# Kernel tuning notes

Measured on AMD Instinct MI355X. Metric: run time of the kernel, lower is better.

## Reference

```python
import jax, jax.numpy as jnp
import numpy as np

TEMPERATURE = 0.5


def setup_inputs() -> dict:
    key = jax.random.key(0)
    k1, k2 = jax.random.split(key)
    B, D = 8192, 128
    z_i = jax.random.normal(k1, (B, D), dtype=jnp.float32)
    z_j = jax.random.normal(k2, (B, D), dtype=jnp.float32)
    return {"z_i": z_i, "z_j": z_j}


def reference(z_i, z_j):
    B = z_i.shape[0]
    eps = 1e-12  # matches torch F.normalize default clamp
    zi = z_i / jnp.maximum(jnp.linalg.norm(z_i, axis=1, keepdims=True), eps)
    zj = z_j / jnp.maximum(jnp.linalg.norm(z_j, axis=1, keepdims=True), eps)
    reps = jnp.concatenate([zi, zj], axis=0)  # [2B, D], unit rows
    # cosine similarity of unit vectors == dot product -> single GEMM
    sim = reps @ reps.T  # [2B, 2B]
    n = 2 * B
    diag = jnp.eye(n, dtype=bool)
    sim = jnp.where(diag, -1e9, sim) / TEMPERATURE
    labels = jnp.concatenate([jnp.arange(B) + B, jnp.arange(B)])  # positive pair indices
    logp = jax.nn.log_softmax(sim, axis=1)
    loss = -jnp.mean(jnp.take_along_axis(logp, labels[:, None], axis=1))
    return loss
```

## Files before the change

### kernel.cpp

```cpp
#include <hip/hip_runtime.h>
#include <hip/hip_bf16.h>

#define NB 8192
#define ND 128
#define N2 16384

#define CPB 512
#define CTILE 64
#define NT (CPB / CTILE)
#define TILEB (CTILE * 128)

typedef __attribute__((ext_vector_type(4))) float f32x4;
typedef __attribute__((ext_vector_type(4))) int v4i;
typedef __attribute__((ext_vector_type(8))) int v8i;

static constexpr float SQRT_C_VAL = 1.69864368f;

__global__ __launch_bounds__(256) void nrm_kernel(const float* __restrict__ zi,
                                                  const float* __restrict__ zj,
                                                  unsigned short* __restrict__ reps8_u16,
                                                  float* __restrict__ pos,
                                                  float* __restrict__ ssum,
                                                  float* __restrict__ sdiag) {
    const int gtid = blockIdx.x * 256 + threadIdx.x;
    if (gtid < N2) ssum[gtid] = 0.f;
    const int pair = gtid >> 6;
    const int lane = threadIdx.x & 63;
    const float2 vi = *reinterpret_cast<const float2*>(zi + pair * ND + lane * 2);
    const float2 vj = *reinterpret_cast<const float2*>(zj + pair * ND + lane * 2);
    float ssi = vi.x * vi.x + vi.y * vi.y;
    float ssj = vj.x * vj.x + vj.y * vj.y;
#pragma unroll
    for (int m = 1; m < 64; m <<= 1) {
        ssi += __shfl_xor(ssi, m);
        ssj += __shfl_xor(ssj, m);
    }
    float ni = fmaxf(sqrtf(ssi), 1e-12f);
    float nj = fmaxf(sqrtf(ssj), 1e-12f);
    const float ii = 1.0f / ni, ij = 1.0f / nj;
    const float uix = vi.x * ii, uiy = vi.y * ii;
    const float ujx = vj.x * ij, ujy = vj.y * ij;
    float d = uix * ujx + uiy * ujy;
#pragma unroll
    for (int m = 1; m < 64; m <<= 1) d += __shfl_xor(d, m);
    if (lane == 0) pos[pair] = d;
    const int pki = __builtin_amdgcn_cvt_pk_fp8_f32(uix * SQRT_C_VAL, uiy * SQRT_C_VAL, 0, false);
    const int pkj = __builtin_amdgcn_cvt_pk_fp8_f32(ujx * SQRT_C_VAL, ujy * SQRT_C_VAL, 0, false);
    reps8_u16[pair * 64 + lane] = (unsigned short)(pki & 0xFFFF);
    reps8_u16[(NB + pair) * 64 + lane] = (unsigned short)(pkj & 0xFFFF);
    const float fi0 = __builtin_amdgcn_cvt_f32_fp8(pki, 0);
    const float fi1 = __builtin_amdgcn_cvt_f32_fp8(pki, 1);
    const float fj0 = __builtin_amdgcn_cvt_f32_fp8(pkj, 0);
    const float fj1 = __builtin_amdgcn_cvt_f32_fp8(pkj, 1);
    float sqi = fi0 * fi0 + fi1 * fi1;
    float sqj = fj0 * fj0 + fj1 * fj1;
#pragma unroll
    for (int m = 1; m < 64; m <<= 1) {
        sqi += __shfl_xor(sqi, m);
        sqj += __shfl_xor(sqj, m);
    }
    if (lane == 0) {
        sdiag[pair] = sqi;
        sdiag[NB + pair] = sqj;
    }
}

__device__ inline void gload_lds16(const void* g, void* l) {
    __builtin_amdgcn_global_load_lds(
        (const __attribute__((address_space(1))) void*)g,
        (__attribute__((address_space(3))) void*)l, 16, 0, 0);
}

__global__ __launch_bounds__(512, 4) void sim_kernel(const char* __restrict__ reps8,
                                                     float* __restrict__ ssum) {
    __shared__ __align__(16) char lds[4][TILEB];
    const int tid = threadIdx.x;
    const int lane = tid & 63;
    const int wid = tid >> 6;
    const int l15 = lane & 15;
    const int l4 = lane >> 4;
    const int rb = blockIdx.x * 256;
    const int cb = blockIdx.y * CPB;
    const int qb = rb + wid * 32;

    v8i qf[2];
#pragma unroll
    for (int g = 0; g < 2; ++g)
        qf[g] = *reinterpret_cast<const v8i*>(
            reps8 + (size_t)(qb + g * 16 + l15) * 128 + l4 * 32);
    __builtin_amdgcn_sched_barrier(0);
    asm volatile("s_waitcnt vmcnt(0)" ::: "memory");
    __builtin_amdgcn_sched_barrier(0);

    f32x4 sacc[2];
#pragma unroll
    for (int g = 0; g < 2; ++g) sacc[g] = {0.f, 0.f, 0.f, 0.f};

    const int m_s = tid >> 4;
    const int sp_s = tid & 15;
    const int s_s = sp_s ^ ((m_s & 3) << 1);
    const char* srcq = reps8 + (size_t)(cb + 2 * m_s + (s_s & 1)) * 128 + (s_s >> 1) * 16;

    auto stage = [&](int t) {
        char* dst = &lds[t & 3][wid * 1024];
        gload_lds16(srcq + (size_t)t * TILEB, dst);
    };

    const int h = l15 >> 1;
    const int sloA = (4 * l4 + (l15 & 1)) ^ ((h & 3) << 1);
    const int rdlo = h * 256 + sloA * 16;
    const int rdhi = h * 256 + (sloA ^ 2) * 16;

    stage(0);
    stage(1);
    stage(2);

#pragma unroll 1
    for (int t = 0; t < NT; ++t) {
        if (t <= NT - 3) {
            asm volatile("s_waitcnt vmcnt(2)" ::: "memory");
        } else if (t == NT - 2) {
            asm volatile("s_waitcnt vmcnt(1)" ::: "memory");
        } else {
            asm volatile("s_waitcnt vmcnt(0)" ::: "memory");
        }
        __builtin_amdgcn_s_barrier();
        if (t + 3 < NT) stage(t + 3);

        const char* lbase = lds[t & 3];
#pragma unroll
        for (int cc = 0; cc < 4; ++cc) {
            const int cg = (cc + wid) & 3;
            const v4i lo = *reinterpret_cast<const v4i*>(lbase + rdlo + cg * 2048);
            const v4i hi = *reinterpret_cast<const v4i*>(lbase + rdhi + cg * 2048);
            const v8i kf = __builtin_shufflevector(lo, hi, 0, 1, 2, 3, 4, 5, 6, 7);
            const f32x4 z4 = {0.f, 0.f, 0.f, 0.f};
            __builtin_amdgcn_s_setprio(1);
            f32x4 acc0 = __builtin_amdgcn_mfma_scale_f32_16x16x128_f8f6f4(
                qf[0], kf, z4, 0, 0, 0, 0x7F7F7F7F, 0, 0x7F7F7F7F);
            f32x4 acc1 = __builtin_amdgcn_mfma_scale_f32_16x16x128_f8f6f4(
                qf[1], kf, z4, 0, 0, 0, 0x7F7F7F7F, 0, 0x7F7F7F7F);
            __builtin_amdgcn_s_setprio(0);
#pragma unroll
            for (int r = 0; r < 4; ++r) {
                sacc[0][r] += __builtin_amdgcn_exp2f(acc0[r]);
                sacc[1][r] += __builtin_amdgcn_exp2f(acc1[r]);
            }
        }
    }

#pragma unroll
    for (int g = 0; g < 2; ++g) {
#pragma unroll
        for (int r = 0; r < 4; ++r) {
#pragma unroll
            for (int m = 1; m < 16; m <<= 1) sacc[g][r] += __shfl_xor(sacc[g][r], m);
        }
    }
    if (l15 == 0) {
#pragma unroll
        for (int g = 0; g < 2; ++g)
#pragma unroll
            for (int r = 0; r < 4; ++r)
                atomicAdd(&ssum[qb + g * 16 + l4 * 4 + r], sacc[g][r]);
    }
}

__global__ __launch_bounds__(1024) void fin_kernel(const float* __restrict__ ssum,
                                                   const float* __restrict__ pos,
                                                   const float* __restrict__ sdiag,
                                                   float* __restrict__ out) {
    const int tid = threadIdx.x;
    float acc = 0.f;
    for (int r = tid; r < N2; r += 1024) {
        const int p = (r < NB) ? r : r - NB;
        acc += logf(ssum[r] - exp2f(sdiag[r])) - 2.0f * pos[p];
    }
#pragma unroll
    for (int m = 1; m < 64; m <<= 1) acc += __shfl_xor(acc, m);
    __shared__ float red[16];
    const int wid = tid >> 6, lane = tid & 63;
    if (lane == 0) red[wid] = acc;
    __syncthreads();
    if (wid == 0) {
        float v = (lane < 16) ? red[lane] : 0.f;
#pragma unroll
        for (int m = 1; m < 16; m <<= 1) v += __shfl_xor(v, m);
        if (lane == 0) out[0] = v / (float)N2;
    }
}

extern "C" void kernel_launch(void* const* d_in, const int* in_sizes, int n_in,
                              void* d_out, int out_size, void* d_ws, size_t ws_size,
                              hipStream_t stream) {
    const float* zi = (const float*)d_in[0];
    const float* zj = (const float*)d_in[1];
    float* out = (float*)d_out;
    char* ws = (char*)d_ws;

    char* reps8 = ws;
    float* pos = (float*)(ws + (size_t)N2 * ND);
    float* ssum = pos + NB;
    float* sdiag = ssum + N2;

    nrm_kernel<<<NB / 4, 256, 0, stream>>>(zi, zj, (unsigned short*)reps8, pos, ssum, sdiag);
    dim3 grid(N2 / 256, N2 / CPB);
    sim_kernel<<<grid, 512, 0, stream>>>(reps8, ssum);
    fin_kernel<<<1, 1024, 0, stream>>>(ssum, pos, sdiag, out);
}
```

Baseline: 57.80 us.

## Exploit similarity-matrix symmetry: compute upper triangle and scatter column sums

The similarity kernel now skips row/column block pairs that lie entirely below the diagonal. Tiles near the diagonal mask out entries with col <= row. Each exponentiated value is added both to its row sum and, through an LDS column-sum buffer plus global atomics, to its column sum, which roughly halves the MFMA and exp2 work. Because the diagonal is now excluded directly, the fp8 diagonal-correction pass and its sdiag buffer are removed. The cost is extra shuffles, LDS atomics and global atomics per tile, uneven work across blocks, and dropping the setprio hints.

```diff
diff --git a/kernel.cpp b/kernel.cpp
--- a/kernel.cpp
+++ b/kernel.cpp
@@ -20,8 +20,7 @@
                                                   const float* __restrict__ zj,
                                                   unsigned short* __restrict__ reps8_u16,
                                                   float* __restrict__ pos,
-                                                  float* __restrict__ ssum,
-                                                  float* __restrict__ sdiag) {
+                                                  float* __restrict__ ssum) {
     const int gtid = blockIdx.x * 256 + threadIdx.x;
     if (gtid < N2) ssum[gtid] = 0.f;
     const int pair = gtid >> 6;
@@ -48,21 +47,6 @@
     const int pkj = __builtin_amdgcn_cvt_pk_fp8_f32(ujx * SQRT_C_VAL, ujy * SQRT_C_VAL, 0, false);
     reps8_u16[pair * 64 + lane] = (unsigned short)(pki & 0xFFFF);
     reps8_u16[(NB + pair) * 64 + lane] = (unsigned short)(pkj & 0xFFFF);
-    const float fi0 = __builtin_amdgcn_cvt_f32_fp8(pki, 0);
-    const float fi1 = __builtin_amdgcn_cvt_f32_fp8(pki, 1);
-    const float fj0 = __builtin_amdgcn_cvt_f32_fp8(pkj, 0);
-    const float fj1 = __builtin_amdgcn_cvt_f32_fp8(pkj, 1);
-    float sqi = fi0 * fi0 + fi1 * fi1;
-    float sqj = fj0 * fj0 + fj1 * fj1;
-#pragma unroll
-    for (int m = 1; m < 64; m <<= 1) {
-        sqi += __shfl_xor(sqi, m);
-        sqj += __shfl_xor(sqj, m);
-    }
-    if (lane == 0) {
-        sdiag[pair] = sqi;
-        sdiag[NB + pair] = sqj;
-    }
 }
 
 __device__ inline void gload_lds16(const void* g, void* l) {
@@ -73,15 +57,23 @@
 
 __global__ __launch_bounds__(512, 4) void sim_kernel(const char* __restrict__ reps8,
                                                      float* __restrict__ ssum) {
+    const int a = blockIdx.x;
+    const int s = blockIdx.y;
+    if (2 * (s + 1) <= a) return;
+
     __shared__ __align__(16) char lds[4][TILEB];
+    __shared__ float cs[CPB];
+
     const int tid = threadIdx.x;
     const int lane = tid & 63;
     const int wid = tid >> 6;
     const int l15 = lane & 15;
     const int l4 = lane >> 4;
-    const int rb = blockIdx.x * 256;
-    const int cb = blockIdx.y * CPB;
+    const int rb = a * 256;
+    const int cb = s * CPB;
     const int qb = rb + wid * 32;
+
+    if (tid < CPB) cs[tid] = 0.f;
 
     v8i qf[2];
 #pragma unroll
@@ -127,6 +119,8 @@
         __builtin_amdgcn_s_barrier();
         if (t + 3 < NT) stage(t + 3);
 
+        const int tc = cb + t * CTILE;
+        const bool msk = (tc <= qb + 31);
         const char* lbase = lds[t & 3];
 #pragma unroll
         for (int cc = 0; cc < 4; ++cc) {
@@ -135,17 +129,37 @@
             const v4i hi = *reinterpret_cast<const v4i*>(lbase + rdhi + cg * 2048);
             const v8i kf = __builtin_shufflevector(lo, hi, 0, 1, 2, 3, 4, 5, 6, 7);
             const f32x4 z4 = {0.f, 0.f, 0.f, 0.f};
-            __builtin_amdgcn_s_setprio(1);
             f32x4 acc0 = __builtin_amdgcn_mfma_scale_f32_16x16x128_f8f6f4(
                 qf[0], kf, z4, 0, 0, 0, 0x7F7F7F7F, 0, 0x7F7F7F7F);
             f32x4 acc1 = __builtin_amdgcn_mfma_scale_f32_16x16x128_f8f6f4(
                 qf[1], kf, z4, 0, 0, 0, 0x7F7F7F7F, 0, 0x7F7F7F7F);
-            __builtin_amdgcn_s_setprio(0);
-#pragma unroll
-            for (int r = 0; r < 4; ++r) {
-                sacc[0][r] += __builtin_amdgcn_exp2f(acc0[r]);
-                sacc[1][r] += __builtin_amdgcn_exp2f(acc1[r]);
+            float csum = 0.f;
+            if (!msk) {
+#pragma unroll
+                for (int r = 0; r < 4; ++r) {
+                    const float e0 = __builtin_amdgcn_exp2f(acc0[r]);
+                    const float e1 = __builtin_amdgcn_exp2f(acc1[r]);
+                    sacc[0][r] += e0;
+                    sacc[1][r] += e1;
+                    csum += e0 + e1;
+                }
+            } else {
+                const int col_abs = tc + cg * 16 + l15;
+                const int row0 = qb + l4 * 4;
+#pragma unroll
+                for (int r = 0; r < 4; ++r) {
+                    float e0 = __builtin_amdgcn_exp2f(acc0[r]);
+                    float e1 = __builtin_amdgcn_exp2f(acc1[r]);
+                    e0 = (col_abs > row0 + r) ? e0 : 0.f;
+                    e1 = (col_abs > row0 + 16 + r) ? e1 : 0.f;
+                    sacc[0][r] += e0;
+                    sacc[1][r] += e1;
+                    csum += e0 + e1;
+                }
             }
+            csum += __shfl_xor(csum, 16);
+            csum += __shfl_xor(csum, 32);
+            if (lane < 16) atomicAdd(&cs[t * CTILE + cg * 16 + lane], csum);
         }
     }
 
@@ -164,17 +178,22 @@
             for (int r = 0; r < 4; ++r)
                 atomicAdd(&ssum[qb + g * 16 + l4 * 4 + r], sacc[g][r]);
     }
+
+    __syncthreads();
+    if (tid < CPB) {
+        const float v = cs[tid];
+        if (v != 0.f) atomicAdd(&ssum[cb + tid], v);
+    }
 }
 
 __global__ __launch_bounds__(1024) void fin_kernel(const float* __restrict__ ssum,
                                                    const float* __restrict__ pos,
-                                                   const float* __restrict__ sdiag,
                                                    float* __restrict__ out) {
     const int tid = threadIdx.x;
     float acc = 0.f;
     for (int r = tid; r < N2; r += 1024) {
         const int p = (r < NB) ? r : r - NB;
-        acc += logf(ssum[r] - exp2f(sdiag[r])) - 2.0f * pos[p];
+        acc += logf(ssum[r]) - 2.0f * pos[p];
     }
 #pragma unroll
     for (int m = 1; m < 64; m <<= 1) acc += __shfl_xor(acc, m);
@@ -201,10 +220,9 @@
     char* reps8 = ws;
     float* pos = (float*)(ws + (size_t)N2 * ND);
     float* ssum = pos + NB;
-    float* sdiag = ssum + N2;
-
-    nrm_kernel<<<NB / 4, 256, 0, stream>>>(zi, zj, (unsigned short*)reps8, pos, ssum, sdiag);
+
+    nrm_kernel<<<NB / 4, 256, 0, stream>>>(zi, zj, (unsigned short*)reps8, pos, ssum);
     dim3 grid(N2 / 256, N2 / CPB);
     sim_kernel<<<grid, 512, 0, stream>>>(reps8, ssum);
-    fin_kernel<<<1, 1024, 0, stream>>>(ssum, pos, sdiag, out);
-}
+    fin_kernel<<<1, 1024, 0, stream>>>(ssum, pos, out);
+}
```

After: 85.57 us. 48.0% more time.
